# Kernel optimization log

Measured on AMD Instinct MI355X. Metric: run time of the kernel, lower is better.

The kernel has to match this reference:

```python
import jax, jax.numpy as jnp
import numpy as np

B, N, FDIM = 8, 2048, 256
ASSIGN_RATIO = 0.1
K = int(N * ASSIGN_RATIO) + 1  # num coarse nodes per graph (205)
DENSITY = 0.01


def setup_inputs() -> dict:
    key = jax.random.key(0)
    k1, k2, k3 = jax.random.split(key, 3)
    x = jax.random.normal(k1, (B, N, FDIM), dtype=jnp.float32)
    u = jax.random.uniform(k2, (B, N, N), dtype=jnp.float32)
    adj = jnp.where(u < DENSITY, u, 0.0)
    adj = 0.5 * (adj + jnp.swapaxes(adj, 1, 2))  # symmetric weighted adjacency
    W = jax.random.normal(k3, (FDIM, 1), dtype=jnp.float32) * 0.05
    b = jnp.zeros((1,), dtype=jnp.float32)
    return {"x": x, "adj": adj, "W": W, "b": b}


def _coarsen(x, adj, W, b):
    I = jnp.eye(N, dtype=adj.dtype)
    # --- GCNConv attention score (self-loops + symmetric normalization) ---
    A_hat = adj + I                       # [B,N,N]
    dg = A_hat.sum(-1) ** -0.5            # deg >= 1 via self-loop
    gcn_norm = dg[:, :, None] * A_hat * dg[:, None, :]
    alpha = jnp.einsum('bnm,bmf,fo->bno', gcn_norm, x, W) + b
    alpha = jax.nn.sigmoid(alpha ** 2)[..., 0]   # [B,N], sigmoid(gcn^2)
    # --- normalize_batch_adj: D^{-1/2}(A+I)D^{-1/2}, zero isolated rows ---
    d = jnp.clip(A_hat.sum(-1), 1.0, None) ** -0.5
    norm_adj = d[:, :, None] * A_hat * d[:, None, :]
    norm_adj = norm_adj * (adj.sum(-1) > 0).astype(adj.dtype)[:, :, None]
    # --- top-k cut on attention ---
    topv, topi = jax.lax.top_k(alpha, K)  # [B,K]
    cut = topv[:, K - 1]                  # k-th largest value per graph
    cut_alpha = jax.nn.relu(alpha + 1e-7 - cut[:, None])   # [B,N]
    # --- assignment matrix S = L1-row-normalized(norm_adj * cut_alpha_cols) ---
    S = norm_adj * cut_alpha[:, None, :]
    S = S / jnp.clip(jnp.abs(S).sum(-1, keepdims=True), 1e-12, None)
    # --- coarsening matmuls ---
    x_c = jnp.einsum('bnm,bnf->bmf', S, x)                 # S^T x
    coarse = jnp.einsum('bnm,bnk,bkl->bml', S, adj, S)     # S^T A S
    coarse = jnp.floor(coarse * 1e4) / 1e4                 # 4-digit truncation
    return x_c, coarse, S, topi


def reference(x, adj, W, b):
    return _coarsen(x, adj, W, b)
```

## Files before the change

kernel.cpp:

```cpp
#include <hip/hip_runtime.h>
#include <cstdint>
#include <cstddef>

#define BB 8
#define NN 2048
#define FD 256
#define KK 205
#define CAP 96
#define SELCAP 256

typedef float f4 __attribute__((ext_vector_type(4)));


__global__ __launch_bounds__(256) void k_spy(const float* __restrict__ adj, const float* __restrict__ x,
                                             const float* __restrict__ W, int2* __restrict__ ell,
                                             int* __restrict__ ell_cnt, float* __restrict__ dg,
                                             float* __restrict__ dgy) {
  int r = blockIdx.x;
  const f4* arow4 = (const f4*)(adj + (size_t)r * NN);
  int t = threadIdx.x;
  int lane = t & 63, wv = t >> 6;
  __shared__ int counter;
  __shared__ float wsum[4], wy[4];
  if (t == 0) counter = 0;
  __syncthreads();
  size_t base = (size_t)r * CAP;
  unsigned long long lmask = (1ull << lane) - 1;
  float ls = 0.f;
#pragma unroll
  for (int j = 0; j < 2; ++j) {
    int i4 = t + j * 256;
    f4 v = __builtin_nontemporal_load(&arow4[i4]);
    int m0 = i4 * 4;
#pragma unroll
    for (int c = 0; c < 4; ++c) {
      float val = v[c];
      unsigned long long mk = __ballot(val != 0.f);
      if (mk) {
        int wbase = 0;
        if (lane == 0) wbase = atomicAdd(&counter, (int)__popcll(mk));
        wbase = __shfl(wbase, 0);
        if (val != 0.f) {
          int p = wbase + (int)__popcll(mk & lmask);
          if (p < CAP) ell[base + p] = make_int2(m0 + c, __float_as_int(val));
        }
      }
      ls += val;
    }
  }
#pragma unroll
  for (int off = 32; off > 0; off >>= 1) ls += __shfl_down(ls, off);
  if (lane == 0) wsum[wv] = ls;
  float xv = x[(size_t)r * FD + t] * W[t];
#pragma unroll
  for (int off = 32; off > 0; off >>= 1) xv += __shfl_down(xv, off);
  if (lane == 0) wy[wv] = xv;
  __syncthreads();
  if (t == 0) {
    int tot = counter; if (tot > CAP) tot = CAP;
    ell_cnt[r] = tot;
    float rs = wsum[0] + wsum[1] + wsum[2] + wsum[3];
    float d = 1.0f / sqrtf(1.0f + rs);
    dg[r] = d;
    dgy[r] = d * (wy[0] + wy[1] + wy[2] + wy[3]);
  }
}

__global__ __launch_bounds__(256) void k_alpha(const int2* __restrict__ ell, const int* __restrict__ ell_cnt,
                                               const float* __restrict__ dg, const float* __restrict__ dgy,
                                               const float* __restrict__ bptr, float* __restrict__ alpha) {
  int lane = threadIdx.x & 63, wv = threadIdx.x >> 6;
  int r = blockIdx.x * 4 + wv;
  int b = r / NN;
  int cnt = ell_cnt[r];
  size_t base = (size_t)r * CAP;
  const float* gyb = dgy + (size_t)b * NN;
  float acc = 0.f;
  for (int j = lane; j < cnt; j += 64) {
    int2 e = ell[base + j];
    acc += __int_as_float(e.y) * gyb[e.x];
  }
#pragma unroll
  for (int off = 32; off > 0; off >>= 1) acc += __shfl_down(acc, off);
  if (lane == 0) {
    float dgn = dg[r];
    float z = dgn * (acc + dgy[r]) + bptr[0];
    float t2 = z * z;
    alpha[r] = 1.0f / (1.0f + expf(-t2));
  }
}

__global__ __launch_bounds__(256) void k_rank(const float* __restrict__ alpha, float* __restrict__ cutv,
                                              float* __restrict__ out_topi, int* __restrict__ sel_cnt) {
  __shared__ unsigned int keys[NN];
  int b = blockIdx.x & 7;
  int chunk = blockIdx.x >> 3;
  int t = threadIdx.x;
  if (chunk == 0 && t == 0) sel_cnt[b] = 0;
  const float* ab = alpha + (size_t)b * NN;
  for (int i = t; i < NN; i += 256) keys[i] = __float_as_uint(ab[i]);
  __syncthreads();
  int i = chunk * 256 + t;
  unsigned int ai = keys[i];
  int rank = 0;
  const uint4* k4 = (const uint4*)keys;
#pragma unroll 4
  for (int j4 = 0; j4 < NN / 4; ++j4) {
    uint4 v = k4[j4];
    int j = j4 * 4;
    rank += (v.x > ai) || (v.x == ai && (j + 0) < i);
    rank += (v.y > ai) || (v.y == ai && (j + 1) < i);
    rank += (v.z > ai) || (v.z == ai && (j + 2) < i);
    rank += (v.w > ai) || (v.w == ai && (j + 3) < i);
  }
  if (rank < KK) out_topi[(size_t)b * KK + rank] = (float)i;
  if (rank == KK - 1) cutv[b] = __uint_as_float(ai);
}

__global__ __launch_bounds__(256) void k_selcut(const float* __restrict__ alpha, const float* __restrict__ cutv,
                                                const float* __restrict__ dg, int2* __restrict__ seldg,
                                                int* __restrict__ sel_list, int* __restrict__ sel_cnt) {
  int r = blockIdx.x * 256 + threadIdx.x;
  int b = r / NN, n = r % NN;
  float ca = fmaxf(alpha[r] + 1e-7f - cutv[b], 0.0f);
  int s = -1;
  if (ca > 0.f) {
    s = atomicAdd(&sel_cnt[b], 1);
    if (s < SELCAP) sel_list[b * SELCAP + s] = n; else s = -1;
  }
  seldg[r] = make_int2(__float_as_int(dg[r] * ca), s);
}

__global__ __launch_bounds__(256) void k_sc(const int2* __restrict__ ell, const int* __restrict__ ell_cnt,
                                            const float* __restrict__ dg, const int2* __restrict__ seldg,
                                            const int* __restrict__ sel_cnt,
                                            float* __restrict__ dginv, float* __restrict__ Sc) {
  int lane = threadIdx.x & 63, wv = threadIdx.x >> 6;
  int r = blockIdx.x * 4 + wv;
  int b = r >> 11, n = r & (NN - 1);
  __shared__ float scrow[4][SELCAP];
  float* sc = scrow[wv];
#pragma unroll
  for (int j = lane; j < SELCAP; j += 64) sc[j] = 0.f;
  int cnt = ell_cnt[r];
  size_t base = (size_t)r * CAP;
  float dgn = dg[r];
  const int2* sdb = seldg + (size_t)b * NN;
  float t0 = 0.f, t1 = 0.f;
  int s0 = -1, s1 = -1;
  if (lane < cnt) {
    int2 e = ell[base + lane];
    int2 sd = sdb[e.x];
    t0 = dgn * __int_as_float(e.y) * __int_as_float(sd.x);
    s0 = sd.y;
  }
  if (lane + 64 < cnt) {
    int2 e = ell[base + lane + 64];
    int2 sd = sdb[e.x];
    t1 = dgn * __int_as_float(e.y) * __int_as_float(sd.x);
    s1 = sd.y;
  }
  float part = t0 + t1;
#pragma unroll
  for (int off = 32; off > 0; off >>= 1) part += __shfl_down(part, off);
  part = __shfl(part, 0);
  int2 sdn = sdb[n];
  float diag = dgn * __int_as_float(sdn.x);
  float rho = part + diag;
  float inv = (cnt > 0) ? (1.0f / fmaxf(rho, 1e-12f)) : 0.f;
  if (lane == 0) dginv[r] = dgn * inv;
  if (s0 >= 0) sc[s0] = t0 * inv;
  if (s1 >= 0) sc[s1] = t1 * inv;
  int nsel = sel_cnt[b]; if (nsel > SELCAP) nsel = SELCAP;
  float dv = diag * inv;
  for (int p = lane; p < nsel; p += 64) {
    float sv = sc[p];
    if (p == sdn.y) sv += dv;
    Sc[(size_t)r * SELCAP + p] = sv;
  }
}

__global__ __launch_bounds__(256) void k_Ms(const int2* __restrict__ ell, const int* __restrict__ ell_cnt,
                                            const int* __restrict__ sel_cnt, const int2* __restrict__ seldg,
                                            const float* __restrict__ dginv, const float* __restrict__ Sc,
                                            float* __restrict__ Mmat, float* __restrict__ outS) {
  int b = blockIdx.x & 7;
  int n = blockIdx.x >> 3;
  int r = b * NN + n;
  int t = threadIdx.x;
  __shared__ float row[NN];
  __shared__ int srk[CAP];
  __shared__ float sav[CAP];
#pragma unroll
  for (int j = 0; j < NN / 256; ++j) row[t + j * 256] = 0.f;
  int cnt = ell_cnt[r];
  size_t base = (size_t)r * CAP;
  float dinv = dginv[r];
  const int2* sdb = seldg + (size_t)b * NN;
  for (int e = t; e < cnt; e += 256) {
    int2 p = ell[base + e];
    srk[e] = b * NN + p.x;
    float v = __int_as_float(p.y);
    sav[e] = v;
    row[p.x] = dinv * v * __int_as_float(sdb[p.x].x);
  }
  __syncthreads();
  float dv = dinv * __int_as_float(sdb[n].x);
  f4* dst = (f4*)(outS + (size_t)r * NN);
  const f4* src = (const f4*)row;
#pragma unroll
  for (int j = 0; j < NN / 4 / 256; ++j) {
    int idx = t + j * 256;
    f4 v = src[idx];
    int b4 = idx * 4;
    v[0] += (b4 + 0 == n) ? dv : 0.f;
    v[1] += (b4 + 1 == n) ? dv : 0.f;
    v[2] += (b4 + 2 == n) ? dv : 0.f;
    v[3] += (b4 + 3 == n) ? dv : 0.f;
    __builtin_nontemporal_store(v, &dst[idx]);
  }
  int nsel = sel_cnt[b]; if (nsel > SELCAP) nsel = SELCAP;
  if (t >= nsel) return;
  float a0 = 0.f, a1 = 0.f, a2 = 0.f, a3 = 0.f, a4 = 0.f, a5 = 0.f, a6 = 0.f, a7 = 0.f;
  int e = 0;
  for (; e + 8 <= cnt; e += 8) {
    a0 += sav[e + 0] * Sc[(size_t)srk[e + 0] * SELCAP + t];
    a1 += sav[e + 1] * Sc[(size_t)srk[e + 1] * SELCAP + t];
    a2 += sav[e + 2] * Sc[(size_t)srk[e + 2] * SELCAP + t];
    a3 += sav[e + 3] * Sc[(size_t)srk[e + 3] * SELCAP + t];
    a4 += sav[e + 4] * Sc[(size_t)srk[e + 4] * SELCAP + t];
    a5 += sav[e + 5] * Sc[(size_t)srk[e + 5] * SELCAP + t];
    a6 += sav[e + 6] * Sc[(size_t)srk[e + 6] * SELCAP + t];
    a7 += sav[e + 7] * Sc[(size_t)srk[e + 7] * SELCAP + t];
  }
  for (; e < cnt; ++e) a0 += sav[e] * Sc[(size_t)srk[e] * SELCAP + t];
  Mmat[(size_t)r * SELCAP + t] = ((a0 + a1) + (a2 + a3)) + ((a4 + a5) + (a6 + a7));
}

__global__ __launch_bounds__(256) void k_epi2(const float* __restrict__ x, const int2* __restrict__ ell,
                                              const int* __restrict__ ell_cnt, const int2* __restrict__ seldg,
                                              const float* __restrict__ dginv, const int* __restrict__ sel_list,
                                              const int* __restrict__ sel_cnt, const float* __restrict__ Mmat,
                                              float* __restrict__ xc, float* __restrict__ coarse) {
  int b = blockIdx.x & 7;
  int m = blockIdx.x >> 3;
  int rm = b * NN + m;
  int t = threadIdx.x;
  __shared__ float row[NN];
  __shared__ int cn[CAP + 1];
  __shared__ float cw[CAP + 1];
  int2 sd_m = seldg[rm];
  bool sel = sd_m.y >= 0;
  if (!sel) {
    f4 z = (f4)(0.f);
    if (t < FD / 4) __builtin_nontemporal_store(z, &((f4*)(xc + (size_t)rm * FD))[t]);
    f4* dco = (f4*)(coarse + (size_t)rm * NN);
    __builtin_nontemporal_store(z, &dco[t]);
    __builtin_nontemporal_store(z, &dco[t + 256]);
    return;
  }
  int nsel = sel_cnt[b]; if (nsel > SELCAP) nsel = SELCAP;
  int cnt = ell_cnt[rm];
#pragma unroll
  for (int j = 0; j < NN / 256; ++j) row[t + j * 256] = 0.f;
  {
    float dgca_m = __int_as_float(sd_m.x);
    for (int j = t; j <= cnt; j += 256) {
      if (j < cnt) {
        int2 e = ell[(size_t)rm * CAP + j];
        cn[j] = b * NN + e.x;
        cw[j] = __int_as_float(e.y) * dgca_m * dginv[b * NN + e.x];
      } else {
        cn[j] = rm;
        cw[j] = dgca_m * dginv[rm];
      }
    }
  }
  __syncthreads();
  bool act = t < nsel;
  float axc = 0.f, aco = 0.f;
  int tot = cnt + 1;
  int e = 0;
  for (; e + 4 <= tot; e += 4) {
    int r0 = cn[e + 0], r1 = cn[e + 1], r2 = cn[e + 2], r3 = cn[e + 3];
    float w0 = cw[e + 0], w1 = cw[e + 1], w2 = cw[e + 2], w3 = cw[e + 3];
    float x0 = x[(size_t)r0 * FD + t];
    float x1 = x[(size_t)r1 * FD + t];
    float x2 = x[(size_t)r2 * FD + t];
    float x3 = x[(size_t)r3 * FD + t];
    float m0 = 0.f, m1 = 0.f, m2 = 0.f, m3 = 0.f;
    if (act) {
      m0 = Mmat[(size_t)r0 * SELCAP + t];
      m1 = Mmat[(size_t)r1 * SELCAP + t];
      m2 = Mmat[(size_t)r2 * SELCAP + t];
      m3 = Mmat[(size_t)r3 * SELCAP + t];
    }
    axc += w0 * x0 + w1 * x1 + w2 * x2 + w3 * x3;
    aco += w0 * m0 + w1 * m1 + w2 * m2 + w3 * m3;
  }
  for (; e < tot; ++e) {
    int rn = cn[e];
    float w = cw[e];
    axc += w * x[(size_t)rn * FD + t];
    if (act) aco += w * Mmat[(size_t)rn * SELCAP + t];
  }
  if (act) row[sel_list[b * SELCAP + t]] = floorf(aco * 10000.0f) / 10000.0f;
  __builtin_nontemporal_store(axc, &xc[(size_t)rm * FD + t]);
  __syncthreads();
  f4* dst = (f4*)(coarse + (size_t)rm * NN);
  const f4* src = (const f4*)row;
#pragma unroll
  for (int j = 0; j < NN / 4 / 256; ++j)
    __builtin_nontemporal_store(src[t + j * 256], &dst[t + j * 256]);
}

extern "C" void kernel_launch(void* const* d_in, const int* in_sizes, int n_in,
                              void* d_out, int out_size, void* d_ws, size_t ws_size,
                              hipStream_t stream) {
  (void)in_sizes; (void)n_in; (void)ws_size; (void)out_size;
  const float* x = (const float*)d_in[0];
  const float* adj = (const float*)d_in[1];
  const float* W = (const float*)d_in[2];
  const float* bptr = (const float*)d_in[3];

  float* out = (float*)d_out;
  const size_t XC_SZ = (size_t)BB * NN * FD;
  const size_t CO_SZ = (size_t)BB * NN * NN;
  const size_t S_SZ  = (size_t)BB * NN * NN;
  float* out_xc = out;
  float* out_co = out + XC_SZ;
  float* out_S  = out + XC_SZ + CO_SZ;
  float* out_ti = out + XC_SZ + CO_SZ + S_SZ;

  char* w = (char*)d_ws;
  int2*  ell     = (int2*)w;  w += (size_t)BB * NN * CAP * 8;
  float* Sc      = (float*)w; w += (size_t)BB * NN * SELCAP * 4;
  float* Mmat    = (float*)w; w += (size_t)BB * NN * SELCAP * 4;
  int2*  seldg   = (int2*)w;  w += (size_t)BB * NN * 8;
  int*   ell_cnt = (int*)w;   w += (size_t)BB * NN * 4;
  float* dg      = (float*)w; w += (size_t)BB * NN * 4;
  float* dgy     = (float*)w; w += (size_t)BB * NN * 4;
  float* alpha   = (float*)w; w += (size_t)BB * NN * 4;
  float* dginv   = (float*)w; w += (size_t)BB * NN * 4;
  float* cutv    = (float*)w; w += (size_t)BB * 4;
  int*   sel_cnt = (int*)w;   w += (size_t)BB * 4;
  int*   sel_list= (int*)w;   w += (size_t)BB * SELCAP * 4;

  k_spy<<<BB * NN, 256, 0, stream>>>(adj, x, W, ell, ell_cnt, dg, dgy);
  k_alpha<<<BB * NN / 4, 256, 0, stream>>>(ell, ell_cnt, dg, dgy, bptr, alpha);
  k_rank<<<BB * 8, 256, 0, stream>>>(alpha, cutv, out_ti, sel_cnt);
  k_selcut<<<BB * NN / 256, 256, 0, stream>>>(alpha, cutv, dg, seldg, sel_list, sel_cnt);
  k_sc<<<BB * NN / 4, 256, 0, stream>>>(ell, ell_cnt, dg, seldg, sel_cnt, dginv, Sc);
  k_Ms<<<BB * NN, 256, 0, stream>>>(ell, ell_cnt, sel_cnt, seldg, dginv, Sc, Mmat, out_S);
  k_epi2<<<BB * NN, 256, 0, stream>>>(x, ell, ell_cnt, seldg, dginv,
                                      sel_list, sel_cnt, Mmat, out_xc, out_co);
}
```

Baseline: 506.2 us.

## Compact epilogue grid to selected nodes; fuse zero-fill into k_Ms; wave-aggregate atomics

Moves the zero-filling of unselected coarse and x_c rows into k_Ms, so k_epi2 launches only BB*SELCAP blocks indexed through sel_list instead of BB*NN blocks that mostly exit early. This removes about 16K near-empty block launches. The selection kernel also replaces per-thread atomics with one wave-level ballot and atomicAdd. The order of sel_list entries is still nondeterministic, and rows past SELCAP rely on the earlier cap behaviour.

```diff
diff --git a/kernel.cpp b/kernel.cpp
--- a/kernel.cpp
+++ b/kernel.cpp
@@ -120,13 +120,23 @@
 __global__ __launch_bounds__(256) void k_selcut(const float* __restrict__ alpha, const float* __restrict__ cutv,
                                                 const float* __restrict__ dg, int2* __restrict__ seldg,
                                                 int* __restrict__ sel_list, int* __restrict__ sel_cnt) {
-  int r = blockIdx.x * 256 + threadIdx.x;
-  int b = r / NN, n = r % NN;
+  int t = threadIdx.x;
+  int r = blockIdx.x * 256 + t;
+  int b = r >> 11, n = r & (NN - 1);
+  int lane = t & 63;
   float ca = fmaxf(alpha[r] + 1e-7f - cutv[b], 0.0f);
+  bool on = ca > 0.f;
+  unsigned long long mk = __ballot(on);
   int s = -1;
-  if (ca > 0.f) {
-    s = atomicAdd(&sel_cnt[b], 1);
-    if (s < SELCAP) sel_list[b * SELCAP + s] = n; else s = -1;
+  if (mk) {
+    int wbase = 0;
+    if (lane == 0) wbase = atomicAdd(&sel_cnt[b], (int)__popcll(mk));
+    wbase = __shfl(wbase, 0);
+    if (on) {
+      unsigned long long lm = (1ull << lane) - 1;
+      s = wbase + (int)__popcll(mk & lm);
+      if (s < SELCAP) sel_list[b * SELCAP + s] = n; else s = -1;
+    }
   }
   seldg[r] = make_int2(__float_as_int(dg[r] * ca), s);
 }
@@ -183,7 +193,8 @@
 __global__ __launch_bounds__(256) void k_Ms(const int2* __restrict__ ell, const int* __restrict__ ell_cnt,
                                             const int* __restrict__ sel_cnt, const int2* __restrict__ seldg,
                                             const float* __restrict__ dginv, const float* __restrict__ Sc,
-                                            float* __restrict__ Mmat, float* __restrict__ outS) {
+                                            float* __restrict__ Mmat, float* __restrict__ outS,
+                                            float* __restrict__ xc, float* __restrict__ coarse) {
   int b = blockIdx.x & 7;
   int n = blockIdx.x >> 3;
   int r = b * NN + n;
@@ -205,7 +216,8 @@
     row[p.x] = dinv * v * __int_as_float(sdb[p.x].x);
   }
   __syncthreads();
-  float dv = dinv * __int_as_float(sdb[n].x);
+  int2 sdn = sdb[n];
+  float dv = dinv * __int_as_float(sdn.x);
   f4* dst = (f4*)(outS + (size_t)r * NN);
   const f4* src = (const f4*)row;
 #pragma unroll
@@ -218,6 +230,13 @@
     v[2] += (b4 + 2 == n) ? dv : 0.f;
     v[3] += (b4 + 3 == n) ? dv : 0.f;
     __builtin_nontemporal_store(v, &dst[idx]);
+  }
+  if (sdn.y < 0) {
+    f4 z = (f4)(0.f);
+    if (t < FD / 4) __builtin_nontemporal_store(z, &((f4*)(xc + (size_t)r * FD))[t]);
+    f4* dco = (f4*)(coarse + (size_t)r * NN);
+    __builtin_nontemporal_store(z, &dco[t]);
+    __builtin_nontemporal_store(z, &dco[t + 256]);
   }
   int nsel = sel_cnt[b]; if (nsel > SELCAP) nsel = SELCAP;
   if (t >= nsel) return;
@@ -243,23 +262,16 @@
                                               const int* __restrict__ sel_cnt, const float* __restrict__ Mmat,
                                               float* __restrict__ xc, float* __restrict__ coarse) {
   int b = blockIdx.x & 7;
-  int m = blockIdx.x >> 3;
+  int si = blockIdx.x >> 3;
+  int nsel = sel_cnt[b]; if (nsel > SELCAP) nsel = SELCAP;
+  if (si >= nsel) return;
+  int m = sel_list[b * SELCAP + si];
   int rm = b * NN + m;
   int t = threadIdx.x;
   __shared__ float row[NN];
   __shared__ int cn[CAP + 1];
   __shared__ float cw[CAP + 1];
   int2 sd_m = seldg[rm];
-  bool sel = sd_m.y >= 0;
-  if (!sel) {
-    f4 z = (f4)(0.f);
-    if (t < FD / 4) __builtin_nontemporal_store(z, &((f4*)(xc + (size_t)rm * FD))[t]);
-    f4* dco = (f4*)(coarse + (size_t)rm * NN);
-    __builtin_nontemporal_store(z, &dco[t]);
-    __builtin_nontemporal_store(z, &dco[t + 256]);
-    return;
-  }
-  int nsel = sel_cnt[b]; if (nsel > SELCAP) nsel = SELCAP;
   int cnt = ell_cnt[rm];
 #pragma unroll
   for (int j = 0; j < NN / 256; ++j) row[t + j * 256] = 0.f;
@@ -351,7 +363,8 @@
   k_rank<<<BB * 8, 256, 0, stream>>>(alpha, cutv, out_ti, sel_cnt);
   k_selcut<<<BB * NN / 256, 256, 0, stream>>>(alpha, cutv, dg, seldg, sel_list, sel_cnt);
   k_sc<<<BB * NN / 4, 256, 0, stream>>>(ell, ell_cnt, dg, seldg, sel_cnt, dginv, Sc);
-  k_Ms<<<BB * NN, 256, 0, stream>>>(ell, ell_cnt, sel_cnt, seldg, dginv, Sc, Mmat, out_S);
-  k_epi2<<<BB * NN, 256, 0, stream>>>(x, ell, ell_cnt, seldg, dginv,
-                                      sel_list, sel_cnt, Mmat, out_xc, out_co);
-}
+  k_Ms<<<BB * NN, 256, 0, stream>>>(ell, ell_cnt, sel_cnt, seldg, dginv, Sc, Mmat,
+                                    out_S, out_xc, out_co);
+  k_epi2<<<BB * SELCAP, 256, 0, stream>>>(x, ell, ell_cnt, seldg, dginv,
+                                          sel_list, sel_cnt, Mmat, out_xc, out_co);
+}
```

New measurement: 480.7 us. 5.0% less time.
